# Kernel tuning notes

Measured on AMD Instinct MI355X. Metric: run time of the kernel, lower is better.

## Reference

```python
import jax, jax.numpy as jnp
import numpy as np

B, T, D, C = 64, 8192, 32, 256  # batch, seq_len, ar_d, data_num_cats


def setup_inputs() -> dict:
    key = jax.random.key(0)
    ks = jax.random.split(key, 8)
    inv = 1.0 / np.sqrt(D)
    return {
        "x": jax.random.randint(ks[0], (B, T), 0, C, dtype=jnp.int32),
        "bos": jax.random.normal(ks[1], (D,), jnp.float32) * 0.01,  # nn.initializers.normal()
        "W_in": jax.random.normal(ks[2], (1, D), jnp.float32),
        "b_in": jnp.zeros((D,), jnp.float32),
        "Wi": jax.random.normal(ks[3], (D, 4 * D), jnp.float32) * inv,
        "Wh": jax.random.normal(ks[4], (D, 4 * D), jnp.float32) * inv,
        "b_lstm": jnp.zeros((4 * D,), jnp.float32),
        "W_out": jax.random.normal(ks[5], (D, C), jnp.float32) * inv,
        "b_out": jnp.zeros((C,), jnp.float32),
    }


def reference(x, bos, W_in, b_in, Wi, Wh, b_lstm, W_out, b_out):
    b, t = x.shape
    d = bos.shape[0]
    # data_preprocess_fn: normalize byte-valued categories to floats
    xf = x.astype(jnp.float32) / 255.0 - 0.5            # [B,T]
    h_in = xf[:, :, None] * W_in[0] + b_in              # Dense(1 -> D): [B,T,D]
    # shift_right with learned bos token
    h_in = jnp.concatenate(
        [jnp.broadcast_to(bos, (b, 1, d)), h_in[:, :-1]], axis=1
    )
    # precompute input contribution to the 4 gates (i,f,g,o) for all steps
    gx = jnp.einsum('btd,dg->btg', h_in, Wi) + b_lstm   # [B,T,4D]
    gx = jnp.swapaxes(gx, 0, 1)                         # [T,B,4D]

    def step(carry, g_in):
        c, h = carry
        g = g_in + h @ Wh                               # [B,4D]
        i, f, gg, o = jnp.split(g, 4, axis=-1)          # flax gate order i,f,g,o
        c = jax.nn.sigmoid(f) * c + jax.nn.sigmoid(i) * jnp.tanh(gg)
        h = jax.nn.sigmoid(o) * jnp.tanh(c)
        return (c, h), h

    init = (jnp.zeros((b, d), gx.dtype), jnp.zeros((b, d), gx.dtype))
    _, hs = jax.lax.scan(step, init, gx)                # [T,B,D]
    hs = jnp.swapaxes(hs, 0, 1)                         # [B,T,D]
    return hs @ W_out + b_out                           # [B,T,C]
```

## Files before the change

### kernel.cpp

```cpp
#include <hip/hip_runtime.h>

#define BB 64
#define TT 8192
#define DD 32
#define GG 128
#define CC 256
#define NC 64
#define CHUNK 128
#define WARM 128

typedef _Float16 half8 __attribute__((ext_vector_type(8)));
typedef float f32x4 __attribute__((ext_vector_type(4)));

__device__ __forceinline__ float fast_exp2(float x) { return __builtin_amdgcn_exp2f(x); }
__device__ __forceinline__ float fast_rcp(float x)  { return __builtin_amdgcn_rcpf(x); }
__device__ __forceinline__ float lane_bcast(float v, int lane) {
    return __int_as_float(__builtin_amdgcn_readlane(__float_as_int(v), lane));
}

__global__ __launch_bounds__(64, 4) void lstm_scan_kernel(
    const int* __restrict__ x, const float* __restrict__ bos,
    const float* __restrict__ W_in, const float* __restrict__ b_in,
    const float* __restrict__ Wi, const float* __restrict__ Wh,
    const float* __restrict__ b_lstm, _Float16* __restrict__ hs)
{
    const int j = threadIdx.x;
    const int blk = blockIdx.x;
    const int b = blk >> 6;
    const int chunk = blk & (NC - 1);
    const int tstart = chunk * CHUNK;
    const int tend = tstart + CHUNK;
    const int t0 = (chunk == 0) ? 0 : (tstart - WARM);
    const bool lolane = (j < 32);
    const int d = j & 31;

    float whA[DD], whB[DD];
#pragma unroll
    for (int k = 0; k < DD; ++k) {
        whA[k] = Wh[k * GG + j];
        whB[k] = Wh[k * GG + j + 64];
    }
    float u0 = 0.f, u1 = 0.f, v0 = 0.f, v1 = 0.f, gb0 = 0.f, gb1 = 0.f;
#pragma unroll
    for (int k = 0; k < DD; ++k) {
        float wiA = Wi[k * GG + j], wiB = Wi[k * GG + j + 64];
        float wv = W_in[k], bv = b_in[k], sv = bos[k];
        u0 = fmaf(wv, wiA, u0);   u1 = fmaf(wv, wiB, u1);
        v0 = fmaf(bv, wiA, v0);   v1 = fmaf(bv, wiB, v1);
        gb0 = fmaf(sv, wiA, gb0); gb1 = fmaf(sv, wiB, gb1);
    }
    {
        float bl0 = b_lstm[j], bl1 = b_lstm[j + 64];
        v0 += bl0; v1 += bl1; gb0 += bl0; gb1 += bl1;
    }

    const float L2E = 1.4426950408889634f;
    const float em = lolane ? (-2.f * L2E) : (-L2E);
    const float sa = lolane ? 2.f : 1.f;
    const float sb = lolane ? -1.f : 0.f;

    float c = 0.f;
    float hv = 0.f;
    float xr = 0.f;

    const int* xb = x + b * TT;
    _Float16* hsb = hs + ((size_t)b * TT) * DD;

    for (int t = t0; t < tend; ++t) {
        if ((t & 63) == 0) {
            int ti = t + j - 1;
            xr = (ti >= 0) ? ((float)xb[ti] * (1.f / 255.f) - 0.5f) : 0.f;
        }
        float xf = lane_bcast(xr, t & 63);
        float a0 = 0.f, a1 = 0.f, a2 = 0.f, a3 = 0.f;
        float c0 = 0.f, c1 = 0.f, c2 = 0.f, c3 = 0.f;
#pragma unroll
        for (int k = 0; k < 8; ++k) {
            float h0 = lane_bcast(hv, k);
            float h1 = lane_bcast(hv, k + 8);
            float h2 = lane_bcast(hv, k + 16);
            float h3 = lane_bcast(hv, k + 24);
            a0 = fmaf(h0, whA[k],      a0);  c0 = fmaf(h0, whB[k],      c0);
            a1 = fmaf(h1, whA[k + 8],  a1);  c1 = fmaf(h1, whB[k + 8],  c1);
            a2 = fmaf(h2, whA[k + 16], a2);  c2 = fmaf(h2, whB[k + 16], c2);
            a3 = fmaf(h3, whA[k + 24], a3);  c3 = fmaf(h3, whB[k + 24], c3);
        }
        float g0 = fmaf(xf, u0, v0) + ((a0 + a1) + (a2 + a3));
        float g1 = fmaf(xf, u1, v1) + ((c0 + c1) + (c2 + c3));
        if (t == 0) { g0 = gb0; g1 = gb1; }
        float e0 = fast_exp2(g0 * (-L2E));
        float s0 = fast_rcp(1.f + e0);
        float e1 = fast_exp2(g1 * em);
        float r1 = fast_rcp(1.f + e1);
        float s1 = fmaf(sa, r1, sb);

        float pm = s0 * s1;
        float valA = lolane ? pm : s0;
        float sw1 = __shfl_xor(valA, 32, 64);
        float sw2 = __shfl_xor(s1, 32, 64);
        float a_t = lolane ? pm : sw1;
        float f_t = lolane ? sw1 : s0;
        float o_t = lolane ? sw2 : s1;
        c = fmaf(f_t, c, a_t);
        float ec = fast_exp2(c * (-2.f * L2E));
        float rc = fast_rcp(1.f + ec);
        float th = fmaf(2.f, rc, -1.f);
        float h = o_t * th;

        if (t >= tstart && lolane) {
            hsb[(size_t)t * DD + d] = (_Float16)h;
        }
        hv = h;
    }
}

__global__ __launch_bounds__(256, 4) void out_gemm_kernel(
    const _Float16* __restrict__ hs, const float* __restrict__ Wo,
    const float* __restrict__ bo, float* __restrict__ out, int nstrips)
{
    __shared__ __align__(16) unsigned char smem[17408];
    _Float16* bfrag = (_Float16*)smem;
    float* bolds = (float*)(smem + 16384);

    for (int i = threadIdx.x; i < DD * CC; i += 256) {
        int k = i >> 8, col = i & 255;
        int ct = col >> 4, c15 = col & 15;
        int Lw = ((k >> 3) << 4) | c15;
        int jj = k & 7;
        bfrag[ct * 512 + Lw * 8 + jj] = (_Float16)Wo[i];
    }
    if (threadIdx.x < CC) bolds[threadIdx.x] = bo[threadIdx.x];
    __syncthreads();

    const int wave = threadIdx.x >> 6;
    const int L = threadIdx.x & 63;
    half8 bf[16];
#pragma unroll
    for (int ct = 0; ct < 16; ++ct)
        bf[ct] = *(const half8*)&bfrag[ct * 512 + L * 8];
    float bcol[16];
#pragma unroll
    for (int ct = 0; ct < 16; ++ct)
        bcol[ct] = bolds[ct * 16 + (L & 15)];
    __syncthreads();

    float* tb = (float*)smem + wave * 1088;

    const int wid = blockIdx.x * 4 + wave;
    const int nw = gridDim.x * 4;
    const int arow_off = (L & 15) * DD + (L >> 4) * 8;
    const int colb = L & 15;
    const int row0 = (L >> 4) * 4;
    for (int s = wid; s < nstrips; s += nw) {
        const _Float16* ap = hs + (size_t)s * 16 * DD;
        half8 af = *(const half8*)(ap + arow_off);
        float* op = out + (size_t)s * 16 * CC;
#pragma unroll
        for (int qq = 0; qq < 4; ++qq) {
#pragma unroll
            for (int ct4 = 0; ct4 < 4; ++ct4) {
                int ct = qq * 4 + ct4;
                f32x4 z = {0.f, 0.f, 0.f, 0.f};
                f32x4 r = __builtin_amdgcn_mfma_f32_16x16x32_f16(af, bf[ct], z, 0, 0, 0);
                float bb = bcol[ct];
#pragma unroll
                for (int rr = 0; rr < 4; ++rr)
                    tb[(row0 + rr) * 68 + ct4 * 16 + colb] = r[rr] + bb;
            }
            __builtin_amdgcn_wave_barrier();
#pragma unroll
            for (int q = 0; q < 4; ++q) {
                int row = q * 4 + (L >> 4);
                float4 v4 = *(const float4*)&tb[row * 68 + (L & 15) * 4];
                *(float4*)&op[(size_t)row * CC + qq * 64 + (L & 15) * 4] = v4;
            }
            __builtin_amdgcn_wave_barrier();
        }
    }
}

extern "C" void kernel_launch(void* const* d_in, const int* in_sizes, int n_in,
                              void* d_out, int out_size, void* d_ws, size_t ws_size,
                              hipStream_t stream) {
    const int*   x      = (const int*)d_in[0];
    const float* bos    = (const float*)d_in[1];
    const float* W_in   = (const float*)d_in[2];
    const float* b_in   = (const float*)d_in[3];
    const float* Wi     = (const float*)d_in[4];
    const float* Wh     = (const float*)d_in[5];
    const float* b_lstm = (const float*)d_in[6];
    const float* W_out  = (const float*)d_in[7];
    const float* b_out  = (const float*)d_in[8];
    float* out = (float*)d_out;
    _Float16* hs = (_Float16*)d_ws;

    lstm_scan_kernel<<<BB * NC, 64, 0, stream>>>(x, bos, W_in, b_in, Wi, Wh, b_lstm, hs);
    out_gemm_kernel<<<2048, 256, 0, stream>>>(hs, W_out, b_out, out, (BB * TT) / 16);
}
```

Measured before the change: 821.3 us.

## Use fp16 dot2 with LDS-broadcast hidden state and longer scan chunks

The recurrent matvec now keeps Wh in packed fp16 pairs and uses fdot2, which halves the FMA count per step. The hidden state is exchanged through a small LDS buffer read as half8 vectors instead of 32 readlane broadcasts. Scan chunks are doubled to 256 steps with 32 chunks per batch, so redundant warmup work drops but each wave's serial chain gets longer and fewer waves run. The output GEMM launch-bounds occupancy hint is lowered, and using fp16 weights and state in the recurrence adds rounding error.

```diff
diff --git a/kernel.cpp b/kernel.cpp
--- a/kernel.cpp
+++ b/kernel.cpp
@@ -5,11 +5,12 @@
 #define DD 32
 #define GG 128
 #define CC 256
-#define NC 64
-#define CHUNK 128
+#define NC 32
+#define CHUNK 256
 #define WARM 128
 
 typedef _Float16 half8 __attribute__((ext_vector_type(8)));
+typedef _Float16 half2t __attribute__((ext_vector_type(2)));
 typedef float f32x4 __attribute__((ext_vector_type(4)));
 
 __device__ __forceinline__ float fast_exp2(float x) { return __builtin_amdgcn_exp2f(x); }
@@ -17,6 +18,16 @@
 __device__ __forceinline__ float lane_bcast(float v, int lane) {
     return __int_as_float(__builtin_amdgcn_readlane(__float_as_int(v), lane));
 }
+
+#if __has_builtin(__builtin_amdgcn_fdot2)
+__device__ __forceinline__ float dot2(half2t a, half2t b, float c) {
+    return __builtin_amdgcn_fdot2(a, b, c, false);
+}
+#else
+__device__ __forceinline__ float dot2(half2t a, half2t b, float c) {
+    return fmaf((float)a[0], (float)b[0], fmaf((float)a[1], (float)b[1], c));
+}
+#endif
 
 __global__ __launch_bounds__(64, 4) void lstm_scan_kernel(
     const int* __restrict__ x, const float* __restrict__ bos,
@@ -26,7 +37,7 @@
 {
     const int j = threadIdx.x;
     const int blk = blockIdx.x;
-    const int b = blk >> 6;
+    const int b = blk >> 5;
     const int chunk = blk & (NC - 1);
     const int tstart = chunk * CHUNK;
     const int tend = tstart + CHUNK;
@@ -34,11 +45,13 @@
     const bool lolane = (j < 32);
     const int d = j & 31;
 
-    float whA[DD], whB[DD];
-#pragma unroll
-    for (int k = 0; k < DD; ++k) {
-        whA[k] = Wh[k * GG + j];
-        whB[k] = Wh[k * GG + j + 64];
+    half2t wA[16], wB[16];
+#pragma unroll
+    for (int p = 0; p < 16; ++p) {
+        wA[p][0] = (_Float16)Wh[(2 * p) * GG + j];
+        wA[p][1] = (_Float16)Wh[(2 * p + 1) * GG + j];
+        wB[p][0] = (_Float16)Wh[(2 * p) * GG + j + 64];
+        wB[p][1] = (_Float16)Wh[(2 * p + 1) * GG + j + 64];
     }
     float u0 = 0.f, u1 = 0.f, v0 = 0.f, v1 = 0.f, gb0 = 0.f, gb1 = 0.f;
 #pragma unroll
@@ -59,9 +72,13 @@
     const float sa = lolane ? 2.f : 1.f;
     const float sb = lolane ? -1.f : 0.f;
 
+    __shared__ __align__(16) _Float16 ldsh[DD];
+
     float c = 0.f;
-    float hv = 0.f;
     float xr = 0.f;
+
+    ldsh[d] = (_Float16)0.f;
+    __builtin_amdgcn_wave_barrier();
 
     const int* xb = x + b * TT;
     _Float16* hsb = hs + ((size_t)b * TT) * DD;
@@ -72,18 +89,31 @@
             xr = (ti >= 0) ? ((float)xb[ti] * (1.f / 255.f) - 0.5f) : 0.f;
         }
         float xf = lane_bcast(xr, t & 63);
+
+        half8 hv0 = *(const half8*)(ldsh + 0);
+        half8 hv1 = *(const half8*)(ldsh + 8);
+        half8 hv2 = *(const half8*)(ldsh + 16);
+        half8 hv3 = *(const half8*)(ldsh + 24);
+        half2t hp[16];
+#pragma unroll
+        for (int r = 0; r < 4; ++r) {
+            hp[r][0]      = hv0[2 * r]; hp[r][1]      = hv0[2 * r + 1];
+            hp[r + 4][0]  = hv1[2 * r]; hp[r + 4][1]  = hv1[2 * r + 1];
+            hp[r + 8][0]  = hv2[2 * r]; hp[r + 8][1]  = hv2[2 * r + 1];
+            hp[r + 12][0] = hv3[2 * r]; hp[r + 12][1] = hv3[2 * r + 1];
+        }
         float a0 = 0.f, a1 = 0.f, a2 = 0.f, a3 = 0.f;
         float c0 = 0.f, c1 = 0.f, c2 = 0.f, c3 = 0.f;
 #pragma unroll
-        for (int k = 0; k < 8; ++k) {
-            float h0 = lane_bcast(hv, k);
-            float h1 = lane_bcast(hv, k + 8);
-            float h2 = lane_bcast(hv, k + 16);
-            float h3 = lane_bcast(hv, k + 24);
-            a0 = fmaf(h0, whA[k],      a0);  c0 = fmaf(h0, whB[k],      c0);
-            a1 = fmaf(h1, whA[k + 8],  a1);  c1 = fmaf(h1, whB[k + 8],  c1);
-            a2 = fmaf(h2, whA[k + 16], a2);  c2 = fmaf(h2, whB[k + 16], c2);
-            a3 = fmaf(h3, whA[k + 24], a3);  c3 = fmaf(h3, whB[k + 24], c3);
+        for (int p = 0; p < 4; ++p) {
+            a0 = dot2(hp[p],      wA[p],      a0);
+            a1 = dot2(hp[p + 4],  wA[p + 4],  a1);
+            a2 = dot2(hp[p + 8],  wA[p + 8],  a2);
+            a3 = dot2(hp[p + 12], wA[p + 12], a3);
+            c0 = dot2(hp[p],      wB[p],      c0);
+            c1 = dot2(hp[p + 4],  wB[p + 4],  c1);
+            c2 = dot2(hp[p + 8],  wB[p + 8],  c2);
+            c3 = dot2(hp[p + 12], wB[p + 12], c3);
         }
         float g0 = fmaf(xf, u0, v0) + ((a0 + a1) + (a2 + a3));
         float g1 = fmaf(xf, u1, v1) + ((c0 + c1) + (c2 + c3));
@@ -107,14 +137,17 @@
         float th = fmaf(2.f, rc, -1.f);
         float h = o_t * th;
 
+        _Float16 h16 = (_Float16)h;
         if (t >= tstart && lolane) {
-            hsb[(size_t)t * DD + d] = (_Float16)h;
-        }
-        hv = h;
-    }
-}
-
-__global__ __launch_bounds__(256, 4) void out_gemm_kernel(
+            hsb[(size_t)t * DD + d] = h16;
+        }
+        __builtin_amdgcn_wave_barrier();
+        ldsh[d] = h16;
+        __builtin_amdgcn_wave_barrier();
+    }
+}
+
+__global__ __launch_bounds__(256, 2) void out_gemm_kernel(
     const _Float16* __restrict__ hs, const float* __restrict__ Wo,
     const float* __restrict__ bo, float* __restrict__ out, int nstrips)
 {
```

Result: faster. 754.7 us (-8.1%).
